# Optimization experiments

Hardware: AMD Instinct MI355X
Metric: run time of the kernel (lower is better)

Reference implementation:

```python
import jax, jax.numpy as jnp
import numpy as np

B = 16384          # batch
D = 1024           # input_size == hidden size of each block
L = 3              # number of hidden blocks (layer_configs)
H, Q = 4, 64       # num_heads, query_size
NKV, V = 128, 256  # num_key_values, value_size  (H*V == D for residual)
OUT = 256          # out_size
EPS = 1e-5


def layernorm(x, g, b):
    m = jnp.mean(x, axis=-1, keepdims=True)
    v = jnp.mean(jnp.square(x - m), axis=-1, keepdims=True)
    return (x - m) * jax.lax.rsqrt(v + EPS) * g + b


def setup_inputs() -> dict:
    key = jax.random.key(0)
    ks = jax.random.split(key, 16)
    scale = 1e-4  # module scales Linear / out_linear weights by 0.0001 at init
    return {
        "x": jax.random.normal(ks[0], (B, D), jnp.float32),
        # per-block Linear (stacked over L identical blocks)
        "W": jax.random.normal(ks[1], (L, D, D), jnp.float32) * scale / np.sqrt(D),
        "b": jax.random.normal(ks[2], (L, D), jnp.float32) * scale,
        # MemLayer params
        "Wq": jax.random.normal(ks[3], (L, H * Q, D), jnp.float32) / np.sqrt(D),
        "keys": jax.random.normal(ks[4], (L, NKV, Q), jnp.float32),
        "values": jax.random.normal(ks[5], (L, NKV, V), jnp.float32),
        "Wout": jax.random.normal(ks[6], (L, D, H * V), jnp.float32) * scale / np.sqrt(H * V),
        # per-block LayerNorm
        "ln_g": jnp.ones((L, D), jnp.float32),
        "ln_b": jnp.zeros((L, D), jnp.float32),
        # final head: Linear(sum(layer_configs)=L*D -> OUT), LayerNorm, Sigmoid
        "Wf": jax.random.normal(ks[7], (OUT, L * D), jnp.float32) * scale / np.sqrt(L * D),
        "bf": jax.random.normal(ks[8], (OUT,), jnp.float32) * scale,
        "lnf_g": jnp.ones((OUT,), jnp.float32),
        "lnf_b": jnp.zeros((OUT,), jnp.float32),
    }


def reference(x, W, b, Wq, keys, values, Wout, ln_g, ln_b, Wf, bf, lnf_g, lnf_b):
    # Dropout layers are identity at inference.
    inv_sqrt_q = 1.0 / np.sqrt(Q).astype(np.float32)
    outs = []
    h = x
    for i in range(L):
        # Linear + ReLU
        h = jax.nn.relu(h @ W[i].T + b[i])
        # MemLayer: scores = einsum('aib,ajb->aijb').sum(-1) == q @ k^T
        q = (h @ Wq[i].T).reshape(B, H, Q)
        scores = jnp.einsum('ahq,nq->ahn', q, keys[i]) * inv_sqrt_q  # (B,H,NKV)
        attn = jax.nn.softmax(scores, axis=-1)
        # einsum('aib,ajc->aijc').mean(axis=2) == attn.sum(-1)[:,:,None] * values.mean(0)
        s = jnp.sum(attn, axis=-1)              # (B,H)
        vmean = jnp.mean(values[i], axis=0)     # (V,)
        mem = (s[:, :, None] * vmean).reshape(B, H * V)
        h = mem @ Wout[i].T + h                 # out_linear + residual
        # LayerNorm (output collected for the final concat)
        h = layernorm(h, ln_g[i], ln_b[i])
        outs.append(h)
    z = jnp.concatenate(outs, axis=-1)          # (B, L*D)
    z = z @ Wf.T + bf
    z = layernorm(z, lnf_g, lnf_b)
    return jax.nn.sigmoid(z)
```

## Files before the change

kernel.cpp:

```cpp
#include <hip/hip_runtime.h>
#include <math.h>

#define EPS 1e-5f

constexpr int Bv   = 16384;
constexpr int Dv   = 1024;
constexpr int Lv   = 3;
constexpr int NKVv = 128;
constexpr int Vv   = 256;
constexpr int OUTv = 256;
constexpr int ZLD  = Lv * Dv;

typedef short bf16x8 __attribute__((ext_vector_type(8)));
typedef float f32x4  __attribute__((ext_vector_type(4)));

using gas_t = __attribute__((address_space(1))) const void;
using las_t = __attribute__((address_space(3))) void;
#define GLD_LDS16(gp, lp) \
    __builtin_amdgcn_global_load_lds((gas_t*)(gp), (las_t*)(lp), 16, 0, 0)

static __device__ __forceinline__ ushort f2bf(float f) {
    unsigned u = __float_as_uint(f);
    u = (u + 0x7fffu + ((u >> 16) & 1u)) >> 16;
    return (ushort)u;
}

__global__ void vmean_kernel(const float* __restrict__ values,
                             float* __restrict__ vmean) {
    const int i = blockIdx.x, t = threadIdx.x;
    const float* vals = values + (size_t)i * NKVv * Vv;
    float s = 0.f;
    for (int n = 0; n < NKVv; ++n) s += vals[n * Vv + t];
    vmean[i * Vv + t] = s * (1.0f / NKVv);
}

__global__ void cvec_kernel(const float* __restrict__ vmean,
                            const float* __restrict__ Wout,
                            float* __restrict__ cvec) {
    const int w = threadIdx.x >> 6, lane = threadIdx.x & 63;
    const int r = blockIdx.x * 8 + w;
    const int i = r >> 10;
    const float4 mv = *(const float4*)&vmean[i * Vv + lane * 4];
    const float* row = Wout + (size_t)r * 1024;
    float acc = 0.f;
#pragma unroll
    for (int c = 0; c < 4; ++c) {
        const float4 rv = *(const float4*)&row[c * 256 + lane * 4];
        acc += mv.x * rv.x + mv.y * rv.y + mv.z * rv.z + mv.w * rv.w;
    }
#pragma unroll
    for (int o = 1; o < 64; o <<= 1) acc += __shfl_xor(acc, o, 64);
    if (lane == 0) cvec[r] = acc;
}

__global__ void conv_wg(const float* __restrict__ W,
                        const float* __restrict__ lng,
                        ushort* __restrict__ out) {
    const int t = blockIdx.x * 256 + threadIdx.x;
    const size_t f = (size_t)t * 8;
    const int i = (int)(f >> 20);
    const int k = (int)(f & 1023);
    const float4 v0 = *(const float4*)&W[f];
    const float4 v1 = *(const float4*)&W[f + 4];
    float4 s0 = make_float4(1.f, 1.f, 1.f, 1.f), s1 = s0;
    if (i > 0) {
        s0 = *(const float4*)&lng[(i - 1) * 1024 + k];
        s1 = *(const float4*)&lng[(i - 1) * 1024 + k + 4];
    }
    ushort4 o0 = {f2bf(v0.x * s0.x), f2bf(v0.y * s0.y), f2bf(v0.z * s0.z), f2bf(v0.w * s0.w)};
    ushort4 o1 = {f2bf(v1.x * s1.x), f2bf(v1.y * s1.y), f2bf(v1.z * s1.z), f2bf(v1.w * s1.w)};
    *(ushort4*)&out[f]     = o0;
    *(ushort4*)&out[f + 4] = o1;
}

__global__ void conv_wfg(const float* __restrict__ Wf,
                         const float* __restrict__ lng,
                         ushort* __restrict__ out) {
    const int t = blockIdx.x * 256 + threadIdx.x;
    const size_t f = (size_t)t * 8;
    const int c = (int)(f % ZLD);
    const float4 v0 = *(const float4*)&Wf[f];
    const float4 v1 = *(const float4*)&Wf[f + 4];
    const float4 s0 = *(const float4*)&lng[c];
    const float4 s1 = *(const float4*)&lng[c + 4];
    ushort4 o0 = {f2bf(v0.x * s0.x), f2bf(v0.y * s0.y), f2bf(v0.z * s0.z), f2bf(v0.w * s0.w)};
    ushort4 o1 = {f2bf(v1.x * s1.x), f2bf(v1.y * s1.y), f2bf(v1.z * s1.z), f2bf(v1.w * s1.w)};
    *(ushort4*)&out[f]     = o0;
    *(ushort4*)&out[f + 4] = o1;
}

__global__ void uv_kernel(const float* __restrict__ W,
                          const float* __restrict__ lng,
                          const float* __restrict__ lnb,
                          float* __restrict__ ub, float* __restrict__ vb) {
    const int w = threadIdx.x >> 6, lane = threadIdx.x & 63;
    const int gw = blockIdx.x * 8 + w;
    const int i = 1 + (gw >> 10), n = gw & 1023;
    const float* Wr = W + ((size_t)i << 20) + ((size_t)n << 10);
    const float* g  = lng + (i - 1) * 1024;
    const float* bb = lnb + (i - 1) * 1024;
    float su = 0.f, sv = 0.f;
#pragma unroll
    for (int c = 0; c < 4; ++c) {
        const int k = c * 256 + lane * 4;
        const float4 wv = *(const float4*)&Wr[k];
        const float4 gv = *(const float4*)&g[k];
        const float4 bv = *(const float4*)&bb[k];
        su += wv.x * gv.x + wv.y * gv.y + wv.z * gv.z + wv.w * gv.w;
        sv += wv.x * bv.x + wv.y * bv.y + wv.z * bv.z + wv.w * bv.w;
    }
#pragma unroll
    for (int o = 1; o < 64; o <<= 1) {
        su += __shfl_xor(su, o, 64);
        sv += __shfl_xor(sv, o, 64);
    }
    if (lane == 0) { ub[(i - 1) * 1024 + n] = su; vb[(i - 1) * 1024 + n] = sv; }
}

__global__ void ufvf_kernel(const float* __restrict__ Wf,
                            const float* __restrict__ lng,
                            const float* __restrict__ lnb,
                            float* __restrict__ uf, float* __restrict__ vf) {
    const int w = threadIdx.x >> 6, lane = threadIdx.x & 63;
    const int gw = blockIdx.x * 8 + w;
    const int i = gw >> 8, n = gw & 255;
    const float* Wr = Wf + (size_t)n * ZLD + i * 1024;
    const float* g  = lng + i * 1024;
    const float* bb = lnb + i * 1024;
    float su = 0.f, sv = 0.f;
#pragma unroll
    for (int c = 0; c < 4; ++c) {
        const int k = c * 256 + lane * 4;
        const float4 wv = *(const float4*)&Wr[k];
        const float4 gv = *(const float4*)&g[k];
        const float4 bv = *(const float4*)&bb[k];
        su += wv.x * gv.x + wv.y * gv.y + wv.z * gv.z + wv.w * gv.w;
        sv += wv.x * bv.x + wv.y * bv.y + wv.z * bv.z + wv.w * bv.w;
    }
#pragma unroll
    for (int o = 1; o < 64; o <<= 1) {
        su += __shfl_xor(su, o, 64);
        sv += __shfl_xor(sv, o, 64);
    }
    if (lane == 0) { uf[i * 256 + n] = su; vf[i * 256 + n] = sv; }
}

__global__ void mr_kernel(const float2* __restrict__ pstats,
                          float2* __restrict__ mr) {
    const int row = blockIdx.x * 256 + threadIdx.x;
    const float4* p = (const float4*)(pstats + ((size_t)row << 4));
    float sum = 0.f, sq = 0.f;
#pragma unroll
    for (int j = 0; j < 8; ++j) {
        const float4 t = p[j];
        sum += t.x + t.z; sq += t.y + t.w;
    }
    const float m = sum * (1.f / Dv);
    const float var = sq * (1.f / Dv) - m * m;
    mr[row] = make_float2(m, rsqrtf(var + EPS));
}

__global__ void conv_x(const float* __restrict__ x, ushort* __restrict__ z) {
    const int t = blockIdx.x * 256 + threadIdx.x;
    const int row = t >> 7, c8 = (t & 127) << 3;
    const float4 v0 = *(const float4*)&x[(size_t)row * 1024 + c8];
    const float4 v1 = *(const float4*)&x[(size_t)row * 1024 + c8 + 4];
    ushort4 o0 = {f2bf(v0.x), f2bf(v0.y), f2bf(v0.z), f2bf(v0.w)};
    ushort4 o1 = {f2bf(v1.x), f2bf(v1.y), f2bf(v1.z), f2bf(v1.w)};
    ushort* p = z + (size_t)row * ZLD + 2048 + c8;
    *(ushort4*)p       = o0;
    *(ushort4*)(p + 4) = o1;
}

#define READ_A(QR, DD)                                                        \
    do { _Pragma("unroll")                                                    \
        for (int mf = 0; mf < 4; ++mf) {                                      \
            const int _o = (DD) * 16384 + (QR) * 8192 + (arow_l + mf * 16) * 64; \
            aR[mf][0] = *(const bf16x8*)&As[_o + ck0];                        \
            aR[mf][1] = *(const bf16x8*)&As[_o + ck1];                        \
        } } while (0)

#define READ_B(QC, DD, BR)                                                    \
    do { _Pragma("unroll")                                                    \
        for (int nf = 0; nf < 2; ++nf) {                                      \
            const int _o = (DD) * 16384 + (QC) * 8192 + (brow_l + nf * 16) * 64; \
            BR[nf][0] = *(const bf16x8*)&Bs[_o + ck0];                        \
            BR[nf][1] = *(const bf16x8*)&Bs[_o + ck1];                        \
        } } while (0)

#define STAGE_A(KT, H, DD)                                                    \
    do { const ushort* _p = gAs + (size_t)((H) * 128 + w16) * lda + (KT) * 64; \
         ushort* _l = As + (DD) * 16384 + (H) * 8192 + w16 * 64;              \
         GLD_LDS16(_p, _l);                                                   \
         GLD_LDS16(_p + (size_t)8 * lda, _l + 512); } while (0)

#define STAGE_B(KT, H, DD)                                                    \
    do { const ushort* _p = gBs + (size_t)((H) * 128 + w16) * ldb + (KT) * 64; \
         ushort* _l = Bs + (DD) * 16384 + (H) * 8192 + w16 * 64;              \
         GLD_LDS16(_p, _l);                                                   \
         GLD_LDS16(_p + (size_t)8 * ldb, _l + 512); } while (0)

#define MFMA_Q(QR, QC, BR)                                                    \
    do { __builtin_amdgcn_s_setprio(1);                                       \
        _Pragma("unroll")                                                     \
        for (int mf = 0; mf < 4; ++mf) {                                      \
            _Pragma("unroll")                                                 \
            for (int nf = 0; nf < 2; ++nf) {                                  \
                acc[QR][QC][mf][nf] = __builtin_amdgcn_mfma_f32_16x16x32_bf16( \
                    aR[mf][0], BR[nf][0], acc[QR][QC][mf][nf], 0, 0, 0);      \
                acc[QR][QC][mf][nf] = __builtin_amdgcn_mfma_f32_16x16x32_bf16( \
                    aR[mf][1], BR[nf][1], acc[QR][QC][mf][nf], 0, 0, 0);      \
            }                                                                 \
        }                                                                     \
        __builtin_amdgcn_s_setprio(0); } while (0)

template<int MODE>
__global__ __launch_bounds__(512, 1)
void gemm256(const ushort* __restrict__ A, int lda,
             const ushort* __restrict__ Bw, int ldb,
             const float* __restrict__ bias,
             const float* __restrict__ cvec,
             const float* __restrict__ u_,
             const float* __restrict__ v_,
             const float2* __restrict__ mrp,
             void* __restrict__ Cv, int ldc,
             int NT, int ksplit,
             float2* __restrict__ pstats) {
    __shared__ __align__(16) char smem[137216];
    ushort* As = (ushort*)smem;
    ushort* Bs = (ushort*)(smem + 65536);
    const int tid  = threadIdx.x;
    const int lane = tid & 63;
    const int w    = tid >> 6;
    const int wr2  = w >> 2, wc2 = w & 3;
    const int w16  = w * 16;

    const int wg  = blockIdx.x;
    const int qchunk = (MODE == 1) ? 24 : 32;
    const int swz = (wg & 7) * qchunk + (wg >> 3);
    const int by  = swz & 63;
    const int bx  = swz >> 6;
    const int m0  = by * 256;
    const int n0  = (MODE == 1) ? 0 : bx * 256;
    const int koff = (MODE == 1) ? bx * ksplit : 0;

    const int swzc = ((lane & 7) ^ ((lane >> 3) & 7)) << 3;
    const ushort* gAs = A  + (size_t)(m0 + (lane >> 3)) * lda + koff + swzc;
    const ushort* gBs = Bw + (size_t)(n0 + (lane >> 3)) * ldb + koff + swzc;

    const int arow_l = wr2 * 64 + (lane & 15);
    const int brow_l = wc2 * 32 + (lane & 15);
    const int ck0 = (((lane >> 4))     ^ (lane & 7)) << 3;
    const int ck1 = ((4 + (lane >> 4)) ^ (lane & 7)) << 3;

    f32x4 acc[2][2][4][2] = {};
    bf16x8 aR[4][2], bR0[2][2], bR1[2][2];

    STAGE_A(0, 0, 0);
    STAGE_B(0, 0, 0);
    STAGE_B(0, 1, 0);
    STAGE_A(0, 1, 0);
    asm volatile("s_waitcnt vmcnt(4)" ::: "memory");
    __builtin_amdgcn_s_barrier();

    for (int t = 0; t < NT; ++t) {
        const int d  = t & 1;
        const int e2 = d ^ 1;
        const bool pf = (t + 1) < NT;
        READ_A(0, d);
        READ_B(0, d, bR0);
        if (pf) STAGE_A(t + 1, 0, e2);
        if (pf) asm volatile("s_waitcnt vmcnt(4)" ::: "memory");
        else    asm volatile("s_waitcnt vmcnt(2)" ::: "memory");
        __builtin_amdgcn_s_barrier();
        MFMA_Q(0, 0, bR0);
        READ_B(1, d, bR1);
        if (pf) STAGE_B(t + 1, 0, e2);
        if (pf) asm volatile("s_waitcnt vmcnt(4)" ::: "memory");
        else    asm volatile("s_waitcnt vmcnt(0)" ::: "memory");
        __builtin_amdgcn_s_barrier();
        MFMA_Q(0, 1, bR1);
        READ_A(1, d);
        if (pf) STAGE_B(t + 1, 1, e2);
        MFMA_Q(1, 1, bR1);
        if (pf) STAGE_A(t + 1, 1, e2);
        if (pf) asm volatile("s_waitcnt vmcnt(4)" ::: "memory");
        __builtin_amdgcn_s_barrier();
        MFMA_Q(1, 0, bR0);
    }

    const int lg4 = (lane >> 4) << 2;
    if (MODE != 1) {
        float bsv[2][2], csv[2][2], uu[2][2], vv[2][2];
#pragma unroll
        for (int qc = 0; qc < 2; ++qc)
#pragma unroll
            for (int nf = 0; nf < 2; ++nf) {
                const int col = n0 + qc * 128 + wc2 * 32 + nf * 16 + (lane & 15);
                bsv[qc][nf] = bias[col];
                csv[qc][nf] = cvec[col];
                if (MODE == 2) { uu[qc][nf] = u_[col]; vv[qc][nf] = v_[col]; }
            }
        __syncthreads();
        float2* mrs = (float2*)smem;
        if (MODE == 2) {
            if (tid < 256) mrs[tid] = mrp[m0 + tid];
            __syncthreads();
        }
#pragma unroll
        for (int qr = 0; qr < 2; ++qr)
#pragma unroll
            for (int mf = 0; mf < 4; ++mf)
#pragma unroll
                for (int r = 0; r < 4; ++r) {
                    const int rloc = qr * 128 + wr2 * 64 + mf * 16 + lg4 + r;
                    float rw = 1.f, rmw = 0.f;
                    if (MODE == 2) {
                        const float2 q = mrs[rloc];
                        rw = q.y; rmw = q.y * q.x;
                    }
                    float sum = 0.f, sq = 0.f;
#pragma unroll
                    for (int qc = 0; qc < 2; ++qc)
#pragma unroll
                        for (int nf = 0; nf < 2; ++nf) {
                            float a = acc[qr][qc][mf][nf][r];
                            float val;
                            if (MODE == 2)
                                val = fmaf(rw, a, fmaf(-rmw, uu[qc][nf],
                                          vv[qc][nf] + bsv[qc][nf]));
                            else
                                val = a + bsv[qc][nf];
                            val = fmaxf(val, 0.f) + csv[qc][nf];
                            acc[qr][qc][mf][nf][r] = val;
                            sum += val; sq += val * val;
                        }
#pragma unroll
                    for (int o = 1; o < 16; o <<= 1) {
                        sum += __shfl_xor(sum, o, 64);
                        sq  += __shfl_xor(sq,  o, 64);
                    }
                    if ((lane & 15) == 0)
                        pstats[(((size_t)(m0 + rloc)) << 4) + (bx << 2) + wc2] =
                            make_float2(sum, sq);
                }
        ushort* tile = (ushort*)(smem + 2048);
#pragma unroll
        for (int qr = 0; qr < 2; ++qr)
#pragma unroll
            for (int qc = 0; qc < 2; ++qc)
#pragma unroll
                for (int mf = 0; mf < 4; ++mf)
#pragma unroll
                    for (int nf = 0; nf < 2; ++nf)
#pragma unroll
                        for (int r = 0; r < 4; ++r) {
                            const int rloc = qr * 128 + wr2 * 64 + mf * 16 + lg4 + r;
                            const int cloc = qc * 128 + wc2 * 32 + nf * 16 + (lane & 15);
                            tile[rloc * 264 + cloc] = f2bf(acc[qr][qc][mf][nf][r]);
                        }
        __syncthreads();
        ushort* C16 = (ushort*)Cv;
        for (int c = tid; c < 256 * 32; c += 512) {
            const int row = c >> 5, ch = (c & 31) << 3;
            const bf16x8 v = *(const bf16x8*)&tile[row * 264 + ch];
            *(bf16x8*)&C16[(size_t)(m0 + row) * ldc + n0 + ch] = v;
        }
    } else {
        const int cbase = lane & 15;
        float* Cb = (float*)Cv + (size_t)bx * ((size_t)Bv * OUTv);
#pragma unroll
        for (int qr = 0; qr < 2; ++qr)
#pragma unroll
            for (int qc = 0; qc < 2; ++qc)
#pragma unroll
                for (int nf = 0; nf < 2; ++nf) {
                    const int col = qc * 128 + wc2 * 32 + nf * 16 + cbase;
#pragma unroll
                    for (int mf = 0; mf < 4; ++mf) {
                        const int row = m0 + qr * 128 + wr2 * 64 + mf * 16 + lg4;
#pragma unroll
                        for (int r = 0; r < 4; ++r)
                            Cb[(size_t)(row + r) * ldc + col] = acc[qr][qc][mf][nf][r];
                    }
                }
    }
}

__global__ void ln_sig_reduce(const float* __restrict__ ps,
                              const float2* __restrict__ mr,
                              const float* __restrict__ uf,
                              const float* __restrict__ vf,
                              const float* __restrict__ bf_,
                              const float* __restrict__ g,
                              const float* __restrict__ bb,
                              float* __restrict__ y) {
    const int lane = threadIdx.x & 63;
    const int row  = blockIdx.x * 4 + (threadIdx.x >> 6);
    const size_t base = (size_t)row * OUTv + lane * 4;
    const size_t SP = (size_t)Bv * OUTv;
    const float2 q0 = mr[row];
    const float2 q1 = mr[Bv + row];
    const float2 q2 = mr[2 * Bv + row];
    const float4 p0 = *(const float4*)&ps[base];
    const float4 p1 = *(const float4*)&ps[base + SP];
    const float4 p2 = *(const float4*)&ps[base + 2 * SP];
    const float4 u0 = *(const float4*)&uf[lane * 4];
    const float4 u1 = *(const float4*)&uf[256 + lane * 4];
    const float4 u2 = *(const float4*)&uf[512 + lane * 4];
    const float4 f0 = *(const float4*)&vf[lane * 4];
    const float4 f1 = *(const float4*)&vf[256 + lane * 4];
    const float4 f2 = *(const float4*)&vf[512 + lane * 4];
    const float4 bv4 = *(const float4*)&bf_[lane * 4];
    const float cst_x = f0.x + f1.x + f2.x + bv4.x;
    const float cst_y = f0.y + f1.y + f2.y + bv4.y;
    const float cst_z = f0.z + f1.z + f2.z + bv4.z;
    const float cst_w = f0.w + f1.w + f2.w + bv4.w;
    const float v0 = q0.y * (p0.x - q0.x * u0.x) + q1.y * (p1.x - q1.x * u1.x)
                   + q2.y * (p2.x - q2.x * u2.x) + cst_x;
    const float v1 = q0.y * (p0.y - q0.x * u0.y) + q1.y * (p1.y - q1.x * u1.y)
                   + q2.y * (p2.y - q2.x * u2.y) + cst_y;
    const float v2 = q0.y * (p0.z - q0.x * u0.z) + q1.y * (p1.z - q1.x * u1.z)
                   + q2.y * (p2.z - q2.x * u2.z) + cst_z;
    const float v3 = q0.y * (p0.w - q0.x * u0.w) + q1.y * (p1.w - q1.x * u1.w)
                   + q2.y * (p2.w - q2.x * u2.w) + cst_w;
    float s = v0 + v1 + v2 + v3;
#pragma unroll
    for (int o = 1; o < 64; o <<= 1) s += __shfl_xor(s, o, 64);
    const float mean = s * (1.f / OUTv);
    const float d0 = v0 - mean, d1 = v1 - mean, d2 = v2 - mean, d3 = v3 - mean;
    float q = d0 * d0 + d1 * d1 + d2 * d2 + d3 * d3;
#pragma unroll
    for (int o = 1; o < 64; o <<= 1) q += __shfl_xor(q, o, 64);
    const float r = rsqrtf(q * (1.f / OUTv) + EPS);
    const float4 gg = *(const float4*)&g[lane * 4];
    const float4 bv = *(const float4*)&bb[lane * 4];
    float4 o;
    const float t0 = d0 * r * gg.x + bv.x;
    const float t1 = d1 * r * gg.y + bv.y;
    const float t2 = d2 * r * gg.z + bv.z;
    const float t3 = d3 * r * gg.w + bv.w;
    o.x = 1.f / (1.f + expf(-t0));
    o.y = 1.f / (1.f + expf(-t1));
    o.z = 1.f / (1.f + expf(-t2));
    o.w = 1.f / (1.f + expf(-t3));
    *(float4*)&y[base] = o;
}

extern "C" void kernel_launch(void* const* d_in, const int* in_sizes, int n_in,
                              void* d_out, int out_size, void* d_ws, size_t ws_size,
                              hipStream_t stream) {
    const float* x      = (const float*)d_in[0];
    const float* W      = (const float*)d_in[1];
    const float* b      = (const float*)d_in[2];
    const float* values = (const float*)d_in[5];
    const float* Wout   = (const float*)d_in[6];
    const float* ln_g   = (const float*)d_in[7];
    const float* ln_b   = (const float*)d_in[8];
    const float* Wf     = (const float*)d_in[9];
    const float* bf     = (const float*)d_in[10];
    const float* lnf_g  = (const float*)d_in[11];
    const float* lnf_b  = (const float*)d_in[12];
    float* out = (float*)d_out;

    char* ws = (char*)d_ws;
    ushort* zbuf = (ushort*)ws;
    ws += (size_t)Bv * ZLD * sizeof(ushort);
    float* psum = (float*)ws;
    ws += (size_t)Bv * Dv * sizeof(float);
    ushort* Wb = (ushort*)ws;
    ws += (size_t)Lv * Dv * Dv * sizeof(ushort);
    ushort* Wfb = (ushort*)ws;
    ws += (size_t)OUTv * ZLD * sizeof(ushort);
    float* cvec = (float*)ws;
    ws += (size_t)Lv * Dv * sizeof(float);
    float* vmean = (float*)ws;
    ws += (size_t)Lv * Vv * sizeof(float);
    float2* pstats = (float2*)ws;
    ws += (size_t)Bv * 16 * sizeof(float2);
    float2* mr3 = (float2*)ws;
    ws += (size_t)3 * Bv * sizeof(float2);
    float* ub = (float*)ws; ws += 2 * Dv * sizeof(float);
    float* vb = (float*)ws; ws += 2 * Dv * sizeof(float);
    float* uf = (float*)ws; ws += 3 * OUTv * sizeof(float);
    float* vf = (float*)ws; ws += 3 * OUTv * sizeof(float);

    conv_wg<<<1536, 256, 0, stream>>>(W, ln_g, Wb);
    conv_wfg<<<384, 256, 0, stream>>>(Wf, ln_g, Wfb);
    conv_x<<<Bv * 128 / 256, 256, 0, stream>>>(x, zbuf);
    vmean_kernel<<<Lv, 256, 0, stream>>>(values, vmean);
    cvec_kernel<<<Lv * Dv / 8, 512, 0, stream>>>(vmean, Wout, cvec);
    uv_kernel<<<256, 512, 0, stream>>>(W, ln_g, ln_b, ub, vb);
    ufvf_kernel<<<96, 512, 0, stream>>>(Wf, ln_g, ln_b, uf, vf);

    gemm256<0><<<dim3(256), 512, 0, stream>>>(
        zbuf + 2048, ZLD, Wb, Dv,
        b, cvec, nullptr, nullptr, nullptr,
        (void*)(zbuf + 0), ZLD, 16, 0, pstats);
    mr_kernel<<<Bv / 256, 256, 0, stream>>>(pstats, mr3);

    for (int i = 1; i < Lv; ++i) {
        gemm256<2><<<dim3(256), 512, 0, stream>>>(
            zbuf + (size_t)(i - 1) * Dv, ZLD, Wb + (size_t)i * Dv * Dv, Dv,
            b + (size_t)i * Dv, cvec + (size_t)i * Dv,
            ub + (size_t)(i - 1) * Dv, vb + (size_t)(i - 1) * Dv,
            mr3 + (size_t)(i - 1) * Bv,
            (void*)(zbuf + (size_t)i * Dv), ZLD, 16, 0, pstats);
        mr_kernel<<<Bv / 256, 256, 0, stream>>>(pstats, mr3 + (size_t)i * Bv);
    }

    gemm256<1><<<dim3(192), 512, 0, stream>>>(
        zbuf, ZLD, Wfb, ZLD, nullptr, nullptr,
        nullptr, nullptr, nullptr,
        (void*)psum, OUTv, 16, 1024, pstats);

    ln_sig_reduce<<<Bv / 4, 256, 0, stream>>>(psum, mr3, uf, vf, bf,
                                              lnf_g, lnf_b, out);
}
```

Before: 218.4 us.

## Fuse row-stat reduction into GEMMs, merge weight prep, store split-K partials as fp16

Removes the separate mr_kernel launches by having each GEMM reduce the previous layer's per-row partial stats in its prologue, with ping-pong pstats buffers and a single block column writing the mean/rstd. The weight conversion and u/v dot-product kernels are merged into per-row wprep/wfprep kernels, so W and Wf are read once. The final split-K GEMM now writes fp16 partials through an LDS tile with coalesced stores instead of scattered fp32 stores, which halves that traffic and lowers precision of the partial sums. This trades fewer launches and less memory traffic for a slightly larger prologue in every GEMM block and fp16 rounding of the partials.

```diff
diff --git a/kernel.cpp b/kernel.cpp
--- a/kernel.cpp
+++ b/kernel.cpp
@@ -23,6 +23,12 @@
     unsigned u = __float_as_uint(f);
     u = (u + 0x7fffu + ((u >> 16) & 1u)) >> 16;
     return (ushort)u;
+}
+static __device__ __forceinline__ ushort f2h(float f) {
+    return __builtin_bit_cast(ushort, (_Float16)f);
+}
+static __device__ __forceinline__ float h2f(ushort u) {
+    return (float)__builtin_bit_cast(_Float16, u);
 }
 
 __global__ void vmean_kernel(const float* __restrict__ values,
@@ -53,111 +59,70 @@
     if (lane == 0) cvec[r] = acc;
 }
 
-__global__ void conv_wg(const float* __restrict__ W,
-                        const float* __restrict__ lng,
-                        ushort* __restrict__ out) {
-    const int t = blockIdx.x * 256 + threadIdx.x;
-    const size_t f = (size_t)t * 8;
-    const int i = (int)(f >> 20);
-    const int k = (int)(f & 1023);
-    const float4 v0 = *(const float4*)&W[f];
-    const float4 v1 = *(const float4*)&W[f + 4];
-    float4 s0 = make_float4(1.f, 1.f, 1.f, 1.f), s1 = s0;
+__global__ void wprep(const float* __restrict__ W,
+                      const float* __restrict__ lng,
+                      const float* __restrict__ lnb,
+                      ushort* __restrict__ Wb,
+                      float* __restrict__ ub, float* __restrict__ vb) {
+    __shared__ float rs[8];
+    const int row = blockIdx.x;
+    const int i = row >> 10, n = row & 1023;
+    const int t = threadIdx.x, lane = t & 63, wv = t >> 6;
+    const float* Wr = W + (size_t)row * 1024;
+    const float4 w4 = *(const float4*)&Wr[t * 4];
+    float4 g4 = make_float4(1.f, 1.f, 1.f, 1.f);
+    float4 b4 = make_float4(0.f, 0.f, 0.f, 0.f);
     if (i > 0) {
-        s0 = *(const float4*)&lng[(i - 1) * 1024 + k];
-        s1 = *(const float4*)&lng[(i - 1) * 1024 + k + 4];
-    }
-    ushort4 o0 = {f2bf(v0.x * s0.x), f2bf(v0.y * s0.y), f2bf(v0.z * s0.z), f2bf(v0.w * s0.w)};
-    ushort4 o1 = {f2bf(v1.x * s1.x), f2bf(v1.y * s1.y), f2bf(v1.z * s1.z), f2bf(v1.w * s1.w)};
-    *(ushort4*)&out[f]     = o0;
-    *(ushort4*)&out[f + 4] = o1;
-}
-
-__global__ void conv_wfg(const float* __restrict__ Wf,
-                         const float* __restrict__ lng,
-                         ushort* __restrict__ out) {
-    const int t = blockIdx.x * 256 + threadIdx.x;
-    const size_t f = (size_t)t * 8;
-    const int c = (int)(f % ZLD);
-    const float4 v0 = *(const float4*)&Wf[f];
-    const float4 v1 = *(const float4*)&Wf[f + 4];
-    const float4 s0 = *(const float4*)&lng[c];
-    const float4 s1 = *(const float4*)&lng[c + 4];
-    ushort4 o0 = {f2bf(v0.x * s0.x), f2bf(v0.y * s0.y), f2bf(v0.z * s0.z), f2bf(v0.w * s0.w)};
-    ushort4 o1 = {f2bf(v1.x * s1.x), f2bf(v1.y * s1.y), f2bf(v1.z * s1.z), f2bf(v1.w * s1.w)};
-    *(ushort4*)&out[f]     = o0;
-    *(ushort4*)&out[f + 4] = o1;
-}
-
-__global__ void uv_kernel(const float* __restrict__ W,
-                          const float* __restrict__ lng,
-                          const float* __restrict__ lnb,
-                          float* __restrict__ ub, float* __restrict__ vb) {
-    const int w = threadIdx.x >> 6, lane = threadIdx.x & 63;
-    const int gw = blockIdx.x * 8 + w;
-    const int i = 1 + (gw >> 10), n = gw & 1023;
-    const float* Wr = W + ((size_t)i << 20) + ((size_t)n << 10);
-    const float* g  = lng + (i - 1) * 1024;
-    const float* bb = lnb + (i - 1) * 1024;
-    float su = 0.f, sv = 0.f;
-#pragma unroll
-    for (int c = 0; c < 4; ++c) {
-        const int k = c * 256 + lane * 4;
-        const float4 wv = *(const float4*)&Wr[k];
-        const float4 gv = *(const float4*)&g[k];
-        const float4 bv = *(const float4*)&bb[k];
-        su += wv.x * gv.x + wv.y * gv.y + wv.z * gv.z + wv.w * gv.w;
-        sv += wv.x * bv.x + wv.y * bv.y + wv.z * bv.z + wv.w * bv.w;
-    }
-#pragma unroll
-    for (int o = 1; o < 64; o <<= 1) {
-        su += __shfl_xor(su, o, 64);
-        sv += __shfl_xor(sv, o, 64);
-    }
-    if (lane == 0) { ub[(i - 1) * 1024 + n] = su; vb[(i - 1) * 1024 + n] = sv; }
-}
-
-__global__ void ufvf_kernel(const float* __restrict__ Wf,
-                            const float* __restrict__ lng,
-                            const float* __restrict__ lnb,
-                            float* __restrict__ uf, float* __restrict__ vf) {
-    const int w = threadIdx.x >> 6, lane = threadIdx.x & 63;
-    const int gw = blockIdx.x * 8 + w;
-    const int i = gw >> 8, n = gw & 255;
-    const float* Wr = Wf + (size_t)n * ZLD + i * 1024;
-    const float* g  = lng + i * 1024;
-    const float* bb = lnb + i * 1024;
-    float su = 0.f, sv = 0.f;
-#pragma unroll
-    for (int c = 0; c < 4; ++c) {
-        const int k = c * 256 + lane * 4;
-        const float4 wv = *(const float4*)&Wr[k];
-        const float4 gv = *(const float4*)&g[k];
-        const float4 bv = *(const float4*)&bb[k];
-        su += wv.x * gv.x + wv.y * gv.y + wv.z * gv.z + wv.w * gv.w;
-        sv += wv.x * bv.x + wv.y * bv.y + wv.z * bv.z + wv.w * bv.w;
-    }
-#pragma unroll
-    for (int o = 1; o < 64; o <<= 1) {
-        su += __shfl_xor(su, o, 64);
-        sv += __shfl_xor(sv, o, 64);
-    }
-    if (lane == 0) { uf[i * 256 + n] = su; vf[i * 256 + n] = sv; }
-}
-
-__global__ void mr_kernel(const float2* __restrict__ pstats,
-                          float2* __restrict__ mr) {
-    const int row = blockIdx.x * 256 + threadIdx.x;
-    const float4* p = (const float4*)(pstats + ((size_t)row << 4));
-    float sum = 0.f, sq = 0.f;
-#pragma unroll
-    for (int j = 0; j < 8; ++j) {
-        const float4 t = p[j];
-        sum += t.x + t.z; sq += t.y + t.w;
-    }
-    const float m = sum * (1.f / Dv);
-    const float var = sq * (1.f / Dv) - m * m;
-    mr[row] = make_float2(m, rsqrtf(var + EPS));
+        g4 = *(const float4*)&lng[(i - 1) * 1024 + t * 4];
+        b4 = *(const float4*)&lnb[(i - 1) * 1024 + t * 4];
+    }
+    const float s0 = w4.x * g4.x, s1 = w4.y * g4.y, s2 = w4.z * g4.z, s3 = w4.w * g4.w;
+    ushort4 o = {f2bf(s0), f2bf(s1), f2bf(s2), f2bf(s3)};
+    *(ushort4*)&Wb[(size_t)row * 1024 + t * 4] = o;
+    float su = s0 + s1 + s2 + s3;
+    float sv = w4.x * b4.x + w4.y * b4.y + w4.z * b4.z + w4.w * b4.w;
+#pragma unroll
+    for (int d = 1; d < 64; d <<= 1) {
+        su += __shfl_xor(su, d, 64);
+        sv += __shfl_xor(sv, d, 64);
+    }
+    if (lane == 0) { rs[wv * 2] = su; rs[wv * 2 + 1] = sv; }
+    __syncthreads();
+    if (t == 0 && i > 0) {
+        ub[(i - 1) * 1024 + n] = rs[0] + rs[2] + rs[4] + rs[6];
+        vb[(i - 1) * 1024 + n] = rs[1] + rs[3] + rs[5] + rs[7];
+    }
+}
+
+__global__ void wfprep(const float* __restrict__ Wf,
+                       const float* __restrict__ lng,
+                       const float* __restrict__ lnb,
+                       ushort* __restrict__ Wfb,
+                       float* __restrict__ uf, float* __restrict__ vf) {
+    __shared__ float rs[8];
+    const int bid = blockIdx.x;
+    const int i = bid >> 8, n = bid & 255;
+    const int t = threadIdx.x, lane = t & 63, wv = t >> 6;
+    const size_t base = (size_t)n * ZLD + i * 1024 + t * 4;
+    const float4 w4 = *(const float4*)&Wf[base];
+    const float4 g4 = *(const float4*)&lng[i * 1024 + t * 4];
+    const float4 b4 = *(const float4*)&lnb[i * 1024 + t * 4];
+    const float s0 = w4.x * g4.x, s1 = w4.y * g4.y, s2 = w4.z * g4.z, s3 = w4.w * g4.w;
+    ushort4 o = {f2bf(s0), f2bf(s1), f2bf(s2), f2bf(s3)};
+    *(ushort4*)&Wfb[base] = o;
+    float su = s0 + s1 + s2 + s3;
+    float sv = w4.x * b4.x + w4.y * b4.y + w4.z * b4.z + w4.w * b4.w;
+#pragma unroll
+    for (int d = 1; d < 64; d <<= 1) {
+        su += __shfl_xor(su, d, 64);
+        sv += __shfl_xor(sv, d, 64);
+    }
+    if (lane == 0) { rs[wv * 2] = su; rs[wv * 2 + 1] = sv; }
+    __syncthreads();
+    if (t == 0) {
+        uf[i * 256 + n] = rs[0] + rs[2] + rs[4] + rs[6];
+        vf[i * 256 + n] = rs[1] + rs[3] + rs[5] + rs[7];
+    }
 }
 
 __global__ void conv_x(const float* __restrict__ x, ushort* __restrict__ z) {
@@ -222,13 +187,15 @@
              const float* __restrict__ cvec,
              const float* __restrict__ u_,
              const float* __restrict__ v_,
-             const float2* __restrict__ mrp,
+             const float2* __restrict__ pstats_in,
+             float2* __restrict__ mrout,
              void* __restrict__ Cv, int ldc,
              int NT, int ksplit,
-             float2* __restrict__ pstats) {
-    __shared__ __align__(16) char smem[137216];
+             float2* __restrict__ pstats_out) {
+    __shared__ __align__(16) char smem[139264];
     ushort* As = (ushort*)smem;
     ushort* Bs = (ushort*)(smem + 65536);
+    float2* mrs = (float2*)(smem + 137216);
     const int tid  = threadIdx.x;
     const int lane = tid & 63;
     const int w    = tid >> 6;
@@ -255,6 +222,23 @@
 
     f32x4 acc[2][2][4][2] = {};
     bf16x8 aR[4][2], bR0[2][2], bR1[2][2];
+
+    const bool doMR = (MODE == 2) || (MODE == 1 && bx == 2);
+    float2 myMR = make_float2(0.f, 0.f);
+    if (doMR && tid < 256) {
+        const float4* pp = (const float4*)(pstats_in + (((size_t)(m0 + tid)) << 4));
+        float sum = 0.f, sq = 0.f;
+#pragma unroll
+        for (int j = 0; j < 8; ++j) {
+            const float4 t4 = pp[j];
+            sum += t4.x + t4.z; sq += t4.y + t4.w;
+        }
+        const float m = sum * (1.f / Dv);
+        const float var = sq * (1.f / Dv) - m * m;
+        myMR = make_float2(m, rsqrtf(var + EPS));
+        if (MODE == 2) mrs[tid] = myMR;
+    }
+    __builtin_amdgcn_sched_barrier(0);
 
     STAGE_A(0, 0, 0);
     STAGE_B(0, 0, 0);
@@ -289,7 +273,10 @@
         MFMA_Q(1, 0, bR0);
     }
 
+    if (doMR && tid < 256 && (MODE == 1 || bx == 0)) mrout[m0 + tid] = myMR;
+
     const int lg4 = (lane >> 4) << 2;
+    ushort* tile = (ushort*)(smem + 2048);
     if (MODE != 1) {
         float bsv[2][2], csv[2][2], uu[2][2], vv[2][2];
 #pragma unroll
@@ -302,11 +289,6 @@
                 if (MODE == 2) { uu[qc][nf] = u_[col]; vv[qc][nf] = v_[col]; }
             }
         __syncthreads();
-        float2* mrs = (float2*)smem;
-        if (MODE == 2) {
-            if (tid < 256) mrs[tid] = mrp[m0 + tid];
-            __syncthreads();
-        }
 #pragma unroll
         for (int qr = 0; qr < 2; ++qr)
 #pragma unroll
@@ -341,10 +323,9 @@
                         sq  += __shfl_xor(sq,  o, 64);
                     }
                     if ((lane & 15) == 0)
-                        pstats[(((size_t)(m0 + rloc)) << 4) + (bx << 2) + wc2] =
+                        pstats_out[(((size_t)(m0 + rloc)) << 4) + (bx << 2) + wc2] =
                             make_float2(sum, sq);
                 }
-        ushort* tile = (ushort*)(smem + 2048);
 #pragma unroll
         for (int qr = 0; qr < 2; ++qr)
 #pragma unroll
@@ -359,35 +340,35 @@
                             const int cloc = qc * 128 + wc2 * 32 + nf * 16 + (lane & 15);
                             tile[rloc * 264 + cloc] = f2bf(acc[qr][qc][mf][nf][r]);
                         }
+    } else {
         __syncthreads();
-        ushort* C16 = (ushort*)Cv;
-        for (int c = tid; c < 256 * 32; c += 512) {
-            const int row = c >> 5, ch = (c & 31) << 3;
-            const bf16x8 v = *(const bf16x8*)&tile[row * 264 + ch];
-            *(bf16x8*)&C16[(size_t)(m0 + row) * ldc + n0 + ch] = v;
-        }
-    } else {
-        const int cbase = lane & 15;
-        float* Cb = (float*)Cv + (size_t)bx * ((size_t)Bv * OUTv);
 #pragma unroll
         for (int qr = 0; qr < 2; ++qr)
 #pragma unroll
             for (int qc = 0; qc < 2; ++qc)
 #pragma unroll
-                for (int nf = 0; nf < 2; ++nf) {
-                    const int col = qc * 128 + wc2 * 32 + nf * 16 + cbase;
-#pragma unroll
-                    for (int mf = 0; mf < 4; ++mf) {
-                        const int row = m0 + qr * 128 + wr2 * 64 + mf * 16 + lg4;
-#pragma unroll
-                        for (int r = 0; r < 4; ++r)
-                            Cb[(size_t)(row + r) * ldc + col] = acc[qr][qc][mf][nf][r];
-                    }
-                }
-    }
-}
-
-__global__ void ln_sig_reduce(const float* __restrict__ ps,
+                for (int mf = 0; mf < 4; ++mf)
+#pragma unroll
+                    for (int nf = 0; nf < 2; ++nf)
+#pragma unroll
+                        for (int r = 0; r < 4; ++r) {
+                            const int rloc = qr * 128 + wr2 * 64 + mf * 16 + lg4 + r;
+                            const int cloc = qc * 128 + wc2 * 32 + nf * 16 + (lane & 15);
+                            tile[rloc * 264 + cloc] = f2h(acc[qr][qc][mf][nf][r]);
+                        }
+    }
+    __syncthreads();
+    ushort* C16 = (MODE == 1)
+        ? ((ushort*)Cv + (size_t)bx * ((size_t)Bv * OUTv))
+        : (ushort*)Cv;
+    for (int c = tid; c < 256 * 32; c += 512) {
+        const int row = c >> 5, ch = (c & 31) << 3;
+        const bf16x8 v = *(const bf16x8*)&tile[row * 264 + ch];
+        *(bf16x8*)&C16[(size_t)(m0 + row) * ldc + n0 + ch] = v;
+    }
+}
+
+__global__ void ln_sig_reduce(const ushort* __restrict__ ps,
                               const float2* __restrict__ mr,
                               const float* __restrict__ uf,
                               const float* __restrict__ vf,
@@ -402,9 +383,9 @@
     const float2 q0 = mr[row];
     const float2 q1 = mr[Bv + row];
     const float2 q2 = mr[2 * Bv + row];
-    const float4 p0 = *(const float4*)&ps[base];
-    const float4 p1 = *(const float4*)&ps[base + SP];
-    const float4 p2 = *(const float4*)&ps[base + 2 * SP];
+    const ushort4 a0 = *(const ushort4*)&ps[base];
+    const ushort4 a1 = *(const ushort4*)&ps[base + SP];
+    const ushort4 a2 = *(const ushort4*)&ps[base + 2 * SP];
     const float4 u0 = *(const float4*)&uf[lane * 4];
     const float4 u1 = *(const float4*)&uf[256 + lane * 4];
     const float4 u2 = *(const float4*)&uf[512 + lane * 4];
@@ -416,14 +397,14 @@
     const float cst_y = f0.y + f1.y + f2.y + bv4.y;
     const float cst_z = f0.z + f1.z + f2.z + bv4.z;
     const float cst_w = f0.w + f1.w + f2.w + bv4.w;
-    const float v0 = q0.y * (p0.x - q0.x * u0.x) + q1.y * (p1.x - q1.x * u1.x)
-                   + q2.y * (p2.x - q2.x * u2.x) + cst_x;
-    const float v1 = q0.y * (p0.y - q0.x * u0.y) + q1.y * (p1.y - q1.x * u1.y)
-                   + q2.y * (p2.y - q2.x * u2.y) + cst_y;
-    const float v2 = q0.y * (p0.z - q0.x * u0.z) + q1.y * (p1.z - q1.x * u1.z)
-                   + q2.y * (p2.z - q2.x * u2.z) + cst_z;
-    const float v3 = q0.y * (p0.w - q0.x * u0.w) + q1.y * (p1.w - q1.x * u1.w)
-                   + q2.y * (p2.w - q2.x * u2.w) + cst_w;
+    const float v0 = q0.y * (h2f(a0.x) - q0.x * u0.x) + q1.y * (h2f(a1.x) - q1.x * u1.x)
+                   + q2.y * (h2f(a2.x) - q2.x * u2.x) + cst_x;
+    const float v1 = q0.y * (h2f(a0.y) - q0.x * u0.y) + q1.y * (h2f(a1.y) - q1.x * u1.y)
+                   + q2.y * (h2f(a2.y) - q2.x * u2.y) + cst_y;
+    const float v2 = q0.y * (h2f(a0.z) - q0.x * u0.z) + q1.y * (h2f(a1.z) - q1.x * u1.z)
+                   + q2.y * (h2f(a2.z) - q2.x * u2.z) + cst_z;
+    const float v3 = q0.y * (h2f(a0.w) - q0.x * u0.w) + q1.y * (h2f(a1.w) - q1.x * u1.w)
+                   + q2.y * (h2f(a2.w) - q2.x * u2.w) + cst_w;
     float s = v0 + v1 + v2 + v3;
 #pragma unroll
     for (int o = 1; o < 64; o <<= 1) s += __shfl_xor(s, o, 64);
@@ -466,8 +447,8 @@
     char* ws = (char*)d_ws;
     ushort* zbuf = (ushort*)ws;
     ws += (size_t)Bv * ZLD * sizeof(ushort);
-    float* psum = (float*)ws;
-    ws += (size_t)Bv * Dv * sizeof(float);
+    ushort* psum = (ushort*)ws;
+    ws += (size_t)3 * Bv * OUTv * sizeof(ushort);
     ushort* Wb = (ushort*)ws;
     ws += (size_t)Lv * Dv * Dv * sizeof(ushort);
     ushort* Wfb = (ushort*)ws;
@@ -476,7 +457,9 @@
     ws += (size_t)Lv * Dv * sizeof(float);
     float* vmean = (float*)ws;
     ws += (size_t)Lv * Vv * sizeof(float);
-    float2* pstats = (float2*)ws;
+    float2* psA = (float2*)ws;
+    ws += (size_t)Bv * 16 * sizeof(float2);
+    float2* psB = (float2*)ws;
     ws += (size_t)Bv * 16 * sizeof(float2);
     float2* mr3 = (float2*)ws;
     ws += (size_t)3 * Bv * sizeof(float2);
@@ -485,34 +468,31 @@
     float* uf = (float*)ws; ws += 3 * OUTv * sizeof(float);
     float* vf = (float*)ws; ws += 3 * OUTv * sizeof(float);
 
-    conv_wg<<<1536, 256, 0, stream>>>(W, ln_g, Wb);
-    conv_wfg<<<384, 256, 0, stream>>>(Wf, ln_g, Wfb);
+    wprep<<<Lv * Dv, 256, 0, stream>>>(W, ln_g, ln_b, Wb, ub, vb);
+    wfprep<<<3 * OUTv, 256, 0, stream>>>(Wf, ln_g, ln_b, Wfb, uf, vf);
     conv_x<<<Bv * 128 / 256, 256, 0, stream>>>(x, zbuf);
     vmean_kernel<<<Lv, 256, 0, stream>>>(values, vmean);
     cvec_kernel<<<Lv * Dv / 8, 512, 0, stream>>>(vmean, Wout, cvec);
-    uv_kernel<<<256, 512, 0, stream>>>(W, ln_g, ln_b, ub, vb);
-    ufvf_kernel<<<96, 512, 0, stream>>>(Wf, ln_g, ln_b, uf, vf);
 
     gemm256<0><<<dim3(256), 512, 0, stream>>>(
         zbuf + 2048, ZLD, Wb, Dv,
-        b, cvec, nullptr, nullptr, nullptr,
-        (void*)(zbuf + 0), ZLD, 16, 0, pstats);
-    mr_kernel<<<Bv / 256, 256, 0, stream>>>(pstats, mr3);
-
-    for (int i = 1; i < Lv; ++i) {
-        gemm256<2><<<dim3(256), 512, 0, stream>>>(
-            zbuf + (size_t)(i - 1) * Dv, ZLD, Wb + (size_t)i * Dv * Dv, Dv,
-            b + (size_t)i * Dv, cvec + (size_t)i * Dv,
-            ub + (size_t)(i - 1) * Dv, vb + (size_t)(i - 1) * Dv,
-            mr3 + (size_t)(i - 1) * Bv,
-            (void*)(zbuf + (size_t)i * Dv), ZLD, 16, 0, pstats);
-        mr_kernel<<<Bv / 256, 256, 0, stream>>>(pstats, mr3 + (size_t)i * Bv);
-    }
+        b, cvec, nullptr, nullptr, nullptr, nullptr,
+        (void*)(zbuf + 0), ZLD, 16, 0, psA);
+
+    gemm256<2><<<dim3(256), 512, 0, stream>>>(
+        zbuf, ZLD, Wb + (size_t)Dv * Dv, Dv,
+        b + Dv, cvec + Dv, ub, vb, psA, mr3,
+        (void*)(zbuf + Dv), ZLD, 16, 0, psB);
+
+    gemm256<2><<<dim3(256), 512, 0, stream>>>(
+        zbuf + Dv, ZLD, Wb + (size_t)2 * Dv * Dv, Dv,
+        b + 2 * Dv, cvec + 2 * Dv, ub + Dv, vb + Dv, psB, mr3 + Bv,
+        (void*)(zbuf + 2 * Dv), ZLD, 16, 0, psA);
 
     gemm256<1><<<dim3(192), 512, 0, stream>>>(
-        zbuf, ZLD, Wfb, ZLD, nullptr, nullptr,
-        nullptr, nullptr, nullptr,
-        (void*)psum, OUTv, 16, 1024, pstats);
+        zbuf, ZLD, Wfb, ZLD, nullptr, nullptr, nullptr, nullptr,
+        psA, mr3 + 2 * Bv,
+        (void*)psum, OUTv, 16, 1024, nullptr);
 
     ln_sig_reduce<<<Bv / 4, 256, 0, stream>>>(psum, mr3, uf, vf, bf,
                                               lnf_g, lnf_b, out);
```

Measured after the change: 205.2 us. -6.0%, faster.
